# Kernel tuning notes

Measured on AMD Instinct MI355X. Metric: run time of the kernel, lower is better.

The kernel has to match this reference:

```python
import jax, jax.numpy as jnp
import numpy as np

N = 100000   # nodes
E = 1600000  # directed edges (avg degree 16)
IN = 256     # input feature dim


def _gcn_norm(src, dst, n):
    # PyG gcn_norm with unit edge weights: deg computed on destination,
    # norm = deg^{-1/2}[src] * deg^{-1/2}[dst]
    deg = jax.ops.segment_sum(jnp.ones_like(dst, jnp.float32), dst, num_segments=n)
    dinv = jnp.where(deg > 0, jax.lax.rsqrt(deg), 0.0)
    return dinv[src] * dinv[dst]


def _gcn_conv(x, W, b, src, dst, norm, n):
    h = x @ W                          # [N, out] dense transform first (PyG order)
    msg = norm[:, None] * h[src]       # gather + scale  [E+N, out]
    agg = jax.ops.segment_sum(msg, dst, num_segments=n)  # scatter-add
    return agg + b


def setup_inputs() -> dict:
    key = jax.random.key(0)
    ks = jax.random.split(key, 5)
    x = jax.random.normal(ks[0], (N, IN), jnp.float32)
    edge_index = jax.random.randint(ks[1], (2, E), 0, N, dtype=jnp.int32)
    W1 = jax.random.normal(ks[2], (IN, 64), jnp.float32) * (1.0 / np.sqrt(IN))
    b1 = jnp.zeros((64,), jnp.float32)
    W2 = jax.random.normal(ks[3], (64, 32), jnp.float32) * (1.0 / np.sqrt(64))
    b2 = jnp.zeros((32,), jnp.float32)
    Wlin = jax.random.normal(ks[4], (32, 1), jnp.float32) * (1.0 / np.sqrt(32))
    blin = jnp.zeros((1,), jnp.float32)
    return {"x": x, "edge_index": edge_index, "W1": W1, "b1": b1,
            "W2": W2, "b2": b2, "Wlin": Wlin, "blin": blin}


def reference(x, edge_index, W1, b1, W2, b2, Wlin, blin):
    n = x.shape[0]
    loops = jnp.arange(n, dtype=edge_index.dtype)  # add self-loops (GCNConv default)
    src = jnp.concatenate([edge_index[0], loops])
    dst = jnp.concatenate([edge_index[1], loops])
    norm = _gcn_norm(src, dst, n)                  # same for both layers
    h = jax.nn.relu(_gcn_conv(x, W1, b1, src, dst, norm, n))
    h = jax.nn.relu(_gcn_conv(h, W2, b2, src, dst, norm, n))
    return h @ Wlin + blin
```

## Files before the change

### kernel.cpp

```cpp
#include <hip/hip_runtime.h>
#include <hip/hip_fp16.h>
#include <math.h>


#define BSH 9

typedef _Float16 half8 __attribute__((ext_vector_type(8)));
typedef float floatx4 __attribute__((ext_vector_type(4)));


static __global__ __launch_bounds__(256) void k_bcount(const int* __restrict__ dst,
                                                       int* __restrict__ bkt_cnt,
                                                       int e, int nbkt) {
    __shared__ int sh[256];
    int t = threadIdx.x;
    sh[t] = 0;
    __syncthreads();
    for (int i = blockIdx.x * 256 + t; i < e; i += gridDim.x * 256)
        atomicAdd(&sh[dst[i] >> BSH], 1);
    __syncthreads();
    if (t < nbkt && sh[t]) atomicAdd(&bkt_cnt[t], sh[t]);
}

static __global__ __launch_bounds__(256) void k_bscan(const int* __restrict__ bkt_cnt,
                                                      int* __restrict__ bkt_off,
                                                      int* __restrict__ bkt_cur,
                                                      int nbkt, int e) {
    __shared__ int sh[256];
    int t = threadIdx.x;
    int v = (t < nbkt) ? bkt_cnt[t] : 0;
    sh[t] = v;
    __syncthreads();
    for (int o = 1; o < 256; o <<= 1) {
        int u = (t >= o) ? sh[t - o] : 0;
        __syncthreads();
        sh[t] += u;
        __syncthreads();
    }
    int excl = sh[t] - v;
    if (t < nbkt) { bkt_off[t] = excl; bkt_cur[t] = excl; }
    if (t == 0) bkt_off[nbkt] = e;
}

static __global__ __launch_bounds__(256) void k_bscatter(const int* __restrict__ src,
                                                         const int* __restrict__ dst,
                                                         int* __restrict__ bkt_cur,
                                                         int* __restrict__ bsrc,
                                                         int* __restrict__ bdst,
                                                         int e, int nbkt) {
    __shared__ int ssrc[4096], sdst[4096];
    __shared__ unsigned char sbkt[4096];
    __shared__ int cnt[256], loff[256], lcur[256], gbase[256], sh[256];
    int t  = threadIdx.x;
    int cb = blockIdx.x * 4096;
    int cc = min(4096, e - cb);

    cnt[t] = 0;
    __syncthreads();
    int es[16], ed[16];
    int nv = 0;
    #pragma unroll
    for (int k = 0; k < 16; ++k) {
        int i = cb + k * 256 + t;
        if (i < e) {
            es[nv] = src[i];
            ed[nv] = dst[i];
            atomicAdd(&cnt[ed[nv] >> BSH], 1);
            ++nv;
        }
    }
    __syncthreads();
    int v = cnt[t];
    sh[t] = v;
    __syncthreads();
    for (int o = 1; o < 256; o <<= 1) {
        int u = (t >= o) ? sh[t - o] : 0;
        __syncthreads();
        sh[t] += u;
        __syncthreads();
    }
    loff[t] = sh[t] - v;
    lcur[t] = sh[t] - v;
    if (t < nbkt && v > 0) gbase[t] = atomicAdd(&bkt_cur[t], v);
    __syncthreads();
    for (int k = 0; k < nv; ++k) {
        int b = ed[k] >> BSH;
        int p = atomicAdd(&lcur[b], 1);
        ssrc[p] = es[k];
        sdst[p] = ed[k];
        sbkt[p] = (unsigned char)b;
    }
    __syncthreads();
    for (int i = t; i < cc; i += 256) {
        int b = sbkt[i];
        int g = gbase[b] + (i - loff[b]);
        bsrc[g] = ssrc[i];
        bdst[g] = sdst[i];
    }
}

static __global__ __launch_bounds__(512) void k_bfinal(const int* __restrict__ bkt_off,
                                                       const int* __restrict__ bsrc,
                                                       const int* __restrict__ bdst,
                                                       float* __restrict__ dinv,
                                                       int* __restrict__ offs,
                                                       int* __restrict__ csr_src, int n) {
    __shared__ int cnt[512], sh[512], lcur[512];
    int t = threadIdx.x;
    int base = blockIdx.x << BSH;
    int e0 = bkt_off[blockIdx.x], e1 = bkt_off[blockIdx.x + 1];
    cnt[t] = 0;
    __syncthreads();
    for (int i = e0 + t; i < e1; i += 512) atomicAdd(&cnt[bdst[i] - base], 1);
    __syncthreads();
    int v = cnt[t];
    if (base + t < n) dinv[base + t] = 1.0f / sqrtf((float)(v + 1));
    sh[t] = v;
    __syncthreads();
    for (int o = 1; o < 512; o <<= 1) {
        int u = (t >= o) ? sh[t - o] : 0;
        __syncthreads();
        sh[t] += u;
        __syncthreads();
    }
    int incl = sh[t];
    if (base + t < n) offs[base + t] = e0 + incl;
    lcur[t] = e0 + incl - v;
    __syncthreads();
    for (int i = e0 + t; i < e1; i += 512) {
        int d = bdst[i] - base;
        int p = atomicAdd(&lcur[d], 1);
        csr_src[p] = bsrc[i];
    }
}

static __global__ __launch_bounds__(256) void k_wfrag(const float* __restrict__ W1,
                                                      _Float16* __restrict__ w1f) {
    int t = threadIdx.x;
    for (int idx = t; idx < 2048; idx += 256) {
        int kb = idx >> 8;
        int nt = (idx >> 6) & 3;
        int l  = idx & 63;
        int k0 = kb * 32 + ((l >> 4) << 3);
        int nn = nt * 16 + (l & 15);
        half8 b;
        #pragma unroll
        for (int j = 0; j < 8; ++j) b[j] = (_Float16)W1[(k0 + j) * 64 + nn];
        *(half8*)(w1f + (size_t)idx * 8) = b;
    }
}

static __global__ __launch_bounds__(256) void k_gemm1m(const float* __restrict__ x,
                                                       const _Float16* __restrict__ w1f,
                                                       _Float16* __restrict__ h1f, int n) {
    __shared__ _Float16 Wl[16384];
    int t = threadIdx.x;
    {
        const float4* s = (const float4*)w1f;
        float4* d = (float4*)Wl;
        #pragma unroll
        for (int i = 0; i < 8; ++i) d[t + i * 256] = s[t + i * 256];
    }
    __syncthreads();

    int l = t & 63;
    int w = t >> 6;
    int r0 = blockIdx.x * 128 + w * 32;
    int kq = (l >> 4) << 3;
    int ra0 = r0 + (l & 15);
    int ra1 = ra0 + 16;
    ra0 = ra0 < n ? ra0 : n - 1;
    ra1 = ra1 < n ? ra1 : n - 1;
    const float* p0 = x + (size_t)ra0 * 256 + kq;
    const float* p1 = x + (size_t)ra1 * 256 + kq;

    floatx4 acc[2][4];
    #pragma unroll
    for (int mt = 0; mt < 2; ++mt)
        #pragma unroll
        for (int nt = 0; nt < 4; ++nt)
            acc[mt][nt] = (floatx4){0.f, 0.f, 0.f, 0.f};

    #pragma unroll
    for (int kb = 0; kb < 8; ++kb) {
        float4 u0 = *(const float4*)(p0 + kb * 32);
        float4 u1 = *(const float4*)(p0 + kb * 32 + 4);
        float4 v0 = *(const float4*)(p1 + kb * 32);
        float4 v1 = *(const float4*)(p1 + kb * 32 + 4);
        half8 a0, a1;
        a0[0] = (_Float16)u0.x; a0[1] = (_Float16)u0.y; a0[2] = (_Float16)u0.z; a0[3] = (_Float16)u0.w;
        a0[4] = (_Float16)u1.x; a0[5] = (_Float16)u1.y; a0[6] = (_Float16)u1.z; a0[7] = (_Float16)u1.w;
        a1[0] = (_Float16)v0.x; a1[1] = (_Float16)v0.y; a1[2] = (_Float16)v0.z; a1[3] = (_Float16)v0.w;
        a1[4] = (_Float16)v1.x; a1[5] = (_Float16)v1.y; a1[6] = (_Float16)v1.z; a1[7] = (_Float16)v1.w;
        #pragma unroll
        for (int nt = 0; nt < 4; ++nt) {
            half8 b = *(const half8*)(Wl + ((size_t)(kb * 4 + nt) * 64 + l) * 8);
            acc[0][nt] = __builtin_amdgcn_mfma_f32_16x16x32_f16(a0, b, acc[0][nt], 0, 0, 0);
            acc[1][nt] = __builtin_amdgcn_mfma_f32_16x16x32_f16(a1, b, acc[1][nt], 0, 0, 0);
        }
    }

    int quad = l >> 4;
    int col  = l & 15;
    #pragma unroll
    for (int mt = 0; mt < 2; ++mt) {
        #pragma unroll
        for (int r = 0; r < 4; ++r) {
            int rr = r0 + mt * 16 + quad * 4 + r;
            if (rr < n) {
                _Float16* o = h1f + (size_t)rr * 64 + col;
                #pragma unroll
                for (int nt = 0; nt < 4; ++nt)
                    o[nt * 16] = (_Float16)acc[mt][nt][r];
            }
        }
    }
}


static __global__ __launch_bounds__(256) void k_agg1gemm2(const int* __restrict__ offs,
                                                          const int* __restrict__ csr_src,
                                                          const float* __restrict__ dinv,
                                                          const __half2* __restrict__ h1h,
                                                          const float* __restrict__ b1,
                                                          const float* __restrict__ W2,
                                                          __half* __restrict__ h2h, int n) {
    __shared__ float Wl[64 * 32];
    __shared__ float aggL[8][64];
    int t = threadIdx.x;
    *(float4*)(Wl + t * 4)        = *(const float4*)(W2 + t * 4);
    *(float4*)(Wl + t * 4 + 1024) = *(const float4*)(W2 + t * 4 + 1024);

    int li = t & 31;
    int ni = t >> 5;
    int node  = blockIdx.x * 8 + ni;
    int nodeC = node < n ? node : n - 1;
    int start = nodeC ? offs[nodeC - 1] : 0;
    int end   = offs[nodeC];
    float dd  = dinv[nodeC];
    float2 hf = __half22float2(h1h[(size_t)nodeC * 32 + li]);
    float accx = dd * hf.x, accy = dd * hf.y;

    int j = start;
    for (; j + 3 < end; j += 4) {
        int s0 = csr_src[j], s1 = csr_src[j + 1], s2 = csr_src[j + 2], s3 = csr_src[j + 3];
        float w0 = dinv[s0], w1 = dinv[s1], w2 = dinv[s2], w3 = dinv[s3];
        float2 v0 = __half22float2(h1h[(size_t)s0 * 32 + li]);
        float2 v1 = __half22float2(h1h[(size_t)s1 * 32 + li]);
        float2 v2 = __half22float2(h1h[(size_t)s2 * 32 + li]);
        float2 v3 = __half22float2(h1h[(size_t)s3 * 32 + li]);
        accx += w0 * v0.x + w1 * v1.x + w2 * v2.x + w3 * v3.x;
        accy += w0 * v0.y + w1 * v1.y + w2 * v2.y + w3 * v3.y;
    }
    for (; j < end; ++j) {
        int s = csr_src[j];
        float w = dinv[s];
        float2 v = __half22float2(h1h[(size_t)s * 32 + li]);
        accx += w * v.x;
        accy += w * v.y;
    }
    float2 bb = ((const float2*)b1)[li];
    aggL[ni][2 * li + 0] = fmaxf(dd * accx + bb.x, 0.f);
    aggL[ni][2 * li + 1] = fmaxf(dd * accy + bb.y, 0.f);
    __syncthreads();

    if (node < n) {
        float s = 0.f;
        #pragma unroll
        for (int k = 0; k < 64; ++k) s += aggL[ni][k] * Wl[k * 32 + li];
        h2h[(size_t)node * 32 + li] = __float2half(s);
    }
}


static __global__ __launch_bounds__(256) void k_gather2f(const int* __restrict__ offs,
                                                         const int* __restrict__ csr_src,
                                                         const float* __restrict__ dinv,
                                                         const __half2* __restrict__ h2h,
                                                         const float* __restrict__ b2,
                                                         const float* __restrict__ Wlin,
                                                         const float* __restrict__ blin,
                                                         float* __restrict__ out, int n) {
    int g    = blockIdx.x * 256 + threadIdx.x;
    int node = g >> 4;
    if (node >= n) return;
    int li = g & 15;
    int start = node ? offs[node - 1] : 0;
    int end   = offs[node];
    float dd  = dinv[node];
    float2 hf = __half22float2(h2h[(size_t)node * 16 + li]);
    float accx = dd * hf.x, accy = dd * hf.y;

    int j = start;
    for (; j + 3 < end; j += 4) {
        int s0 = csr_src[j], s1 = csr_src[j + 1], s2 = csr_src[j + 2], s3 = csr_src[j + 3];
        float w0 = dinv[s0], w1 = dinv[s1], w2 = dinv[s2], w3 = dinv[s3];
        float2 v0 = __half22float2(h2h[(size_t)s0 * 16 + li]);
        float2 v1 = __half22float2(h2h[(size_t)s1 * 16 + li]);
        float2 v2 = __half22float2(h2h[(size_t)s2 * 16 + li]);
        float2 v3 = __half22float2(h2h[(size_t)s3 * 16 + li]);
        accx += w0 * v0.x + w1 * v1.x + w2 * v2.x + w3 * v3.x;
        accy += w0 * v0.y + w1 * v1.y + w2 * v2.y + w3 * v3.y;
    }
    for (; j < end; ++j) {
        int s = csr_src[j];
        float w = dinv[s];
        float2 v = __half22float2(h2h[(size_t)s * 16 + li]);
        accx += w * v.x;
        accy += w * v.y;
    }
    float2 bb = ((const float2*)b2)[li];
    float2 wl = ((const float2*)Wlin)[li];
    float val = fmaxf(dd * accx + bb.x, 0.f) * wl.x +
                fmaxf(dd * accy + bb.y, 0.f) * wl.y;
    #pragma unroll
    for (int m = 8; m >= 1; m >>= 1) val += __shfl_xor(val, m);
    if (li == 0) out[node] = val + blin[0];
}

extern "C" void kernel_launch(void* const* d_in, const int* in_sizes, int n_in,
                              void* d_out, int out_size, void* d_ws, size_t ws_size,
                              hipStream_t stream) {
    const float* x    = (const float*)d_in[0];
    const int*   ei   = (const int*)d_in[1];
    const float* W1   = (const float*)d_in[2];
    const float* b1   = (const float*)d_in[3];
    const float* W2   = (const float*)d_in[4];
    const float* b2   = (const float*)d_in[5];
    const float* Wlin = (const float*)d_in[6];
    const float* blin = (const float*)d_in[7];
    float* out = (float*)d_out;

    const int n = in_sizes[0] / 256;
    const int e = in_sizes[1] / 2;
    const int* src = ei;
    const int* dst = ei + e;
    const int nbkt = (n + 511) >> BSH;

    char* wp = (char*)d_ws;
    __half2*  h1h = (__half2*)wp;
    _Float16* h1f = (_Float16*)wp;    wp += (size_t)n * 32 * 4;
    __half*   h2h = (__half*)wp;      wp += (size_t)n * 32 * 2;
    float*    dinv = (float*)wp;      wp += (size_t)n * 4;
    int*      offs = (int*)wp;        wp += (size_t)n * 4;
    int*      csr_src = (int*)wp;     wp += (size_t)e * 4;
    int*      bsrc = (int*)wp;        wp += (size_t)e * 4;
    int*      bdst = (int*)wp;        wp += (size_t)e * 4;
    int*      bkt_cnt = (int*)wp;     wp += 256 * 4;
    int*      bkt_off = (int*)wp;     wp += 257 * 4;
    int*      bkt_cur = (int*)wp;     wp += 256 * 4;
    _Float16* w1f = (_Float16*)wp;

    dim3 B(256);
    hipMemsetAsync(bkt_cnt, 0, (size_t)nbkt * 4, stream);
    k_bcount  <<<256, B, 0, stream>>>(dst, bkt_cnt, e, nbkt);
    k_bscan   <<<1, B, 0, stream>>>(bkt_cnt, bkt_off, bkt_cur, nbkt, e);
    k_bscatter<<<(e + 4095) / 4096, B, 0, stream>>>(src, dst, bkt_cur, bsrc, bdst, e, nbkt);
    k_bfinal  <<<nbkt, 512, 0, stream>>>(bkt_off, bsrc, bdst, dinv, offs, csr_src, n);

    k_wfrag   <<<1, B, 0, stream>>>(W1, w1f);
    k_gemm1m  <<<(n + 127) / 128, B, 0, stream>>>(x, w1f, h1f, n);
    k_agg1gemm2<<<(n + 7) / 8, B, 0, stream>>>(offs, csr_src, dinv, h1h, b1, W2, h2h, n);
    k_gather2f <<<(n * 16 + 255) / 256, B, 0, stream>>>(offs, csr_src, dinv, (const __half2*)h2h,
                                                        b2, Wlin, blin, out, n);
}
```

Baseline: 333.1 us.

## Fuse edge bucketing with first GEMM and use fixed-capacity buckets

Result: faster. 294.9 us (-11.5%).

```diff
diff --git a/kernel.cpp b/kernel.cpp
--- a/kernel.cpp
+++ b/kernel.cpp
@@ -3,136 +3,11 @@
 #include <math.h>
 
 
-#define BSH 9
+#define BSH  9
+#define BCAP 12288
 
 typedef _Float16 half8 __attribute__((ext_vector_type(8)));
 typedef float floatx4 __attribute__((ext_vector_type(4)));
-
-
-static __global__ __launch_bounds__(256) void k_bcount(const int* __restrict__ dst,
-                                                       int* __restrict__ bkt_cnt,
-                                                       int e, int nbkt) {
-    __shared__ int sh[256];
-    int t = threadIdx.x;
-    sh[t] = 0;
-    __syncthreads();
-    for (int i = blockIdx.x * 256 + t; i < e; i += gridDim.x * 256)
-        atomicAdd(&sh[dst[i] >> BSH], 1);
-    __syncthreads();
-    if (t < nbkt && sh[t]) atomicAdd(&bkt_cnt[t], sh[t]);
-}
-
-static __global__ __launch_bounds__(256) void k_bscan(const int* __restrict__ bkt_cnt,
-                                                      int* __restrict__ bkt_off,
-                                                      int* __restrict__ bkt_cur,
-                                                      int nbkt, int e) {
-    __shared__ int sh[256];
-    int t = threadIdx.x;
-    int v = (t < nbkt) ? bkt_cnt[t] : 0;
-    sh[t] = v;
-    __syncthreads();
-    for (int o = 1; o < 256; o <<= 1) {
-        int u = (t >= o) ? sh[t - o] : 0;
-        __syncthreads();
-        sh[t] += u;
-        __syncthreads();
-    }
-    int excl = sh[t] - v;
-    if (t < nbkt) { bkt_off[t] = excl; bkt_cur[t] = excl; }
-    if (t == 0) bkt_off[nbkt] = e;
-}
-
-static __global__ __launch_bounds__(256) void k_bscatter(const int* __restrict__ src,
-                                                         const int* __restrict__ dst,
-                                                         int* __restrict__ bkt_cur,
-                                                         int* __restrict__ bsrc,
-                                                         int* __restrict__ bdst,
-                                                         int e, int nbkt) {
-    __shared__ int ssrc[4096], sdst[4096];
-    __shared__ unsigned char sbkt[4096];
-    __shared__ int cnt[256], loff[256], lcur[256], gbase[256], sh[256];
-    int t  = threadIdx.x;
-    int cb = blockIdx.x * 4096;
-    int cc = min(4096, e - cb);
-
-    cnt[t] = 0;
-    __syncthreads();
-    int es[16], ed[16];
-    int nv = 0;
-    #pragma unroll
-    for (int k = 0; k < 16; ++k) {
-        int i = cb + k * 256 + t;
-        if (i < e) {
-            es[nv] = src[i];
-            ed[nv] = dst[i];
-            atomicAdd(&cnt[ed[nv] >> BSH], 1);
-            ++nv;
-        }
-    }
-    __syncthreads();
-    int v = cnt[t];
-    sh[t] = v;
-    __syncthreads();
-    for (int o = 1; o < 256; o <<= 1) {
-        int u = (t >= o) ? sh[t - o] : 0;
-        __syncthreads();
-        sh[t] += u;
-        __syncthreads();
-    }
-    loff[t] = sh[t] - v;
-    lcur[t] = sh[t] - v;
-    if (t < nbkt && v > 0) gbase[t] = atomicAdd(&bkt_cur[t], v);
-    __syncthreads();
-    for (int k = 0; k < nv; ++k) {
-        int b = ed[k] >> BSH;
-        int p = atomicAdd(&lcur[b], 1);
-        ssrc[p] = es[k];
-        sdst[p] = ed[k];
-        sbkt[p] = (unsigned char)b;
-    }
-    __syncthreads();
-    for (int i = t; i < cc; i += 256) {
-        int b = sbkt[i];
-        int g = gbase[b] + (i - loff[b]);
-        bsrc[g] = ssrc[i];
-        bdst[g] = sdst[i];
-    }
-}
-
-static __global__ __launch_bounds__(512) void k_bfinal(const int* __restrict__ bkt_off,
-                                                       const int* __restrict__ bsrc,
-                                                       const int* __restrict__ bdst,
-                                                       float* __restrict__ dinv,
-                                                       int* __restrict__ offs,
-                                                       int* __restrict__ csr_src, int n) {
-    __shared__ int cnt[512], sh[512], lcur[512];
-    int t = threadIdx.x;
-    int base = blockIdx.x << BSH;
-    int e0 = bkt_off[blockIdx.x], e1 = bkt_off[blockIdx.x + 1];
-    cnt[t] = 0;
-    __syncthreads();
-    for (int i = e0 + t; i < e1; i += 512) atomicAdd(&cnt[bdst[i] - base], 1);
-    __syncthreads();
-    int v = cnt[t];
-    if (base + t < n) dinv[base + t] = 1.0f / sqrtf((float)(v + 1));
-    sh[t] = v;
-    __syncthreads();
-    for (int o = 1; o < 512; o <<= 1) {
-        int u = (t >= o) ? sh[t - o] : 0;
-        __syncthreads();
-        sh[t] += u;
-        __syncthreads();
-    }
-    int incl = sh[t];
-    if (base + t < n) offs[base + t] = e0 + incl;
-    lcur[t] = e0 + incl - v;
-    __syncthreads();
-    for (int i = e0 + t; i < e1; i += 512) {
-        int d = bdst[i] - base;
-        int p = atomicAdd(&lcur[d], 1);
-        csr_src[p] = bsrc[i];
-    }
-}
 
 static __global__ __launch_bounds__(256) void k_wfrag(const float* __restrict__ W1,
                                                       _Float16* __restrict__ w1f) {
@@ -150,73 +25,169 @@
     }
 }
 
-static __global__ __launch_bounds__(256) void k_gemm1m(const float* __restrict__ x,
-                                                       const _Float16* __restrict__ w1f,
-                                                       _Float16* __restrict__ h1f, int n) {
-    __shared__ _Float16 Wl[16384];
+static __global__ __launch_bounds__(256) void k_fat(const float* __restrict__ x,
+                                                    const _Float16* __restrict__ w1f,
+                                                    _Float16* __restrict__ h1f,
+                                                    const int* __restrict__ src,
+                                                    const int* __restrict__ dst,
+                                                    int* __restrict__ bkt_cnt,
+                                                    int* __restrict__ epack,
+                                                    int n, int e, int nScat) {
+    __shared__ alignas(16) char smem[32768];
     int t = threadIdx.x;
-    {
-        const float4* s = (const float4*)w1f;
-        float4* d = (float4*)Wl;
-        #pragma unroll
-        for (int i = 0; i < 8; ++i) d[t + i * 256] = s[t + i * 256];
-    }
-    __syncthreads();
-
-    int l = t & 63;
-    int w = t >> 6;
-    int r0 = blockIdx.x * 128 + w * 32;
-    int kq = (l >> 4) << 3;
-    int ra0 = r0 + (l & 15);
-    int ra1 = ra0 + 16;
-    ra0 = ra0 < n ? ra0 : n - 1;
-    ra1 = ra1 < n ? ra1 : n - 1;
-    const float* p0 = x + (size_t)ra0 * 256 + kq;
-    const float* p1 = x + (size_t)ra1 * 256 + kq;
-
-    floatx4 acc[2][4];
-    #pragma unroll
-    for (int mt = 0; mt < 2; ++mt)
-        #pragma unroll
-        for (int nt = 0; nt < 4; ++nt)
-            acc[mt][nt] = (floatx4){0.f, 0.f, 0.f, 0.f};
-
-    #pragma unroll
-    for (int kb = 0; kb < 8; ++kb) {
-        float4 u0 = *(const float4*)(p0 + kb * 32);
-        float4 u1 = *(const float4*)(p0 + kb * 32 + 4);
-        float4 v0 = *(const float4*)(p1 + kb * 32);
-        float4 v1 = *(const float4*)(p1 + kb * 32 + 4);
-        half8 a0, a1;
-        a0[0] = (_Float16)u0.x; a0[1] = (_Float16)u0.y; a0[2] = (_Float16)u0.z; a0[3] = (_Float16)u0.w;
-        a0[4] = (_Float16)u1.x; a0[5] = (_Float16)u1.y; a0[6] = (_Float16)u1.z; a0[7] = (_Float16)u1.w;
-        a1[0] = (_Float16)v0.x; a1[1] = (_Float16)v0.y; a1[2] = (_Float16)v0.z; a1[3] = (_Float16)v0.w;
-        a1[4] = (_Float16)v1.x; a1[5] = (_Float16)v1.y; a1[6] = (_Float16)v1.z; a1[7] = (_Float16)v1.w;
-        #pragma unroll
-        for (int nt = 0; nt < 4; ++nt) {
-            half8 b = *(const half8*)(Wl + ((size_t)(kb * 4 + nt) * 64 + l) * 8);
-            acc[0][nt] = __builtin_amdgcn_mfma_f32_16x16x32_f16(a0, b, acc[0][nt], 0, 0, 0);
-            acc[1][nt] = __builtin_amdgcn_mfma_f32_16x16x32_f16(a1, b, acc[1][nt], 0, 0, 0);
-        }
-    }
-
-    int quad = l >> 4;
-    int col  = l & 15;
-    #pragma unroll
-    for (int mt = 0; mt < 2; ++mt) {
-        #pragma unroll
-        for (int r = 0; r < 4; ++r) {
-            int rr = r0 + mt * 16 + quad * 4 + r;
-            if (rr < n) {
-                _Float16* o = h1f + (size_t)rr * 64 + col;
-                #pragma unroll
-                for (int nt = 0; nt < 4; ++nt)
-                    o[nt * 16] = (_Float16)acc[mt][nt][r];
+
+    if ((int)blockIdx.x < nScat) {
+        int*           sp    = (int*)smem;
+        unsigned char* sbkt  = (unsigned char*)(smem + 16384);
+        int*           cnt   = (int*)(smem + 20480);
+        int*           loff  = (int*)(smem + 21504);
+        int*           lcur  = (int*)(smem + 22528);
+        int*           gbase = (int*)(smem + 23552);
+        int*           sh    = (int*)(smem + 24576);
+        int cb = blockIdx.x * 4096;
+        int cc = min(4096, e - cb);
+
+        cnt[t] = 0;
+        __syncthreads();
+        int ep[16]; unsigned char eb[16];
+        int nv = 0;
+        #pragma unroll
+        for (int k = 0; k < 16; ++k) {
+            int i = cb + k * 256 + t;
+            if (i < e) {
+                int s = src[i], d = dst[i];
+                int b = d >> BSH;
+                ep[nv] = ((d & 511) << 17) | s;
+                eb[nv] = (unsigned char)b;
+                atomicAdd(&cnt[b], 1);
+                ++nv;
             }
         }
-    }
-}
-
+        __syncthreads();
+        int v = cnt[t];
+        sh[t] = v;
+        __syncthreads();
+        for (int o = 1; o < 256; o <<= 1) {
+            int u = (t >= o) ? sh[t - o] : 0;
+            __syncthreads();
+            sh[t] += u;
+            __syncthreads();
+        }
+        loff[t] = sh[t] - v;
+        lcur[t] = sh[t] - v;
+        if (v > 0) gbase[t] = t * BCAP + atomicAdd(&bkt_cnt[t], v);
+        __syncthreads();
+        for (int k = 0; k < nv; ++k) {
+            int b = eb[k];
+            int p = atomicAdd(&lcur[b], 1);
+            sp[p] = ep[k];
+            sbkt[p] = (unsigned char)b;
+        }
+        __syncthreads();
+        for (int i = t; i < cc; i += 256) {
+            int b = sbkt[i];
+            epack[gbase[b] + (i - loff[b])] = sp[i];
+        }
+    } else {
+        _Float16* Wl = (_Float16*)smem;
+        {
+            const float4* s = (const float4*)w1f;
+            float4* d = (float4*)smem;
+            #pragma unroll
+            for (int i = 0; i < 8; ++i) d[t + i * 256] = s[t + i * 256];
+        }
+        __syncthreads();
+
+        int l = t & 63;
+        int w = t >> 6;
+        int r0 = (blockIdx.x - nScat) * 128 + w * 32;
+        int kq = (l >> 4) << 3;
+        int ra0 = r0 + (l & 15);
+        int ra1 = ra0 + 16;
+        ra0 = ra0 < n ? ra0 : n - 1;
+        ra1 = ra1 < n ? ra1 : n - 1;
+        const float* p0 = x + (size_t)ra0 * 256 + kq;
+        const float* p1 = x + (size_t)ra1 * 256 + kq;
+
+        floatx4 acc[2][4];
+        #pragma unroll
+        for (int mt = 0; mt < 2; ++mt)
+            #pragma unroll
+            for (int nt = 0; nt < 4; ++nt)
+                acc[mt][nt] = (floatx4){0.f, 0.f, 0.f, 0.f};
+
+        #pragma unroll
+        for (int kb = 0; kb < 8; ++kb) {
+            float4 u0 = *(const float4*)(p0 + kb * 32);
+            float4 u1 = *(const float4*)(p0 + kb * 32 + 4);
+            float4 v0 = *(const float4*)(p1 + kb * 32);
+            float4 v1 = *(const float4*)(p1 + kb * 32 + 4);
+            half8 a0, a1;
+            a0[0] = (_Float16)u0.x; a0[1] = (_Float16)u0.y; a0[2] = (_Float16)u0.z; a0[3] = (_Float16)u0.w;
+            a0[4] = (_Float16)u1.x; a0[5] = (_Float16)u1.y; a0[6] = (_Float16)u1.z; a0[7] = (_Float16)u1.w;
+            a1[0] = (_Float16)v0.x; a1[1] = (_Float16)v0.y; a1[2] = (_Float16)v0.z; a1[3] = (_Float16)v0.w;
+            a1[4] = (_Float16)v1.x; a1[5] = (_Float16)v1.y; a1[6] = (_Float16)v1.z; a1[7] = (_Float16)v1.w;
+            #pragma unroll
+            for (int nt = 0; nt < 4; ++nt) {
+                half8 b = *(const half8*)(Wl + ((size_t)(kb * 4 + nt) * 64 + l) * 8);
+                acc[0][nt] = __builtin_amdgcn_mfma_f32_16x16x32_f16(a0, b, acc[0][nt], 0, 0, 0);
+                acc[1][nt] = __builtin_amdgcn_mfma_f32_16x16x32_f16(a1, b, acc[1][nt], 0, 0, 0);
+            }
+        }
+
+        int quad = l >> 4;
+        int col  = l & 15;
+        #pragma unroll
+        for (int mt = 0; mt < 2; ++mt) {
+            #pragma unroll
+            for (int r = 0; r < 4; ++r) {
+                int rr = r0 + mt * 16 + quad * 4 + r;
+                if (rr < n) {
+                    _Float16* o = h1f + (size_t)rr * 64 + col;
+                    #pragma unroll
+                    for (int nt = 0; nt < 4; ++nt)
+                        o[nt * 16] = (_Float16)acc[mt][nt][r];
+                }
+            }
+        }
+    }
+}
+
+static __global__ __launch_bounds__(512) void k_bfinal(const int* __restrict__ bkt_cnt,
+                                                       const int* __restrict__ epack,
+                                                       float* __restrict__ dinv,
+                                                       int* __restrict__ offs,
+                                                       int* __restrict__ csr_src, int n) {
+    __shared__ int cnt[512], sh[512], lcur[512];
+    int t = threadIdx.x;
+    int base = blockIdx.x << BSH;
+    int e0 = blockIdx.x * BCAP;
+    int e1 = e0 + bkt_cnt[blockIdx.x];
+    cnt[t] = 0;
+    __syncthreads();
+    for (int i = e0 + t; i < e1; i += 512) atomicAdd(&cnt[epack[i] >> 17], 1);
+    __syncthreads();
+    int v = cnt[t];
+    if (base + t < n) dinv[base + t] = 1.0f / sqrtf((float)(v + 1));
+    sh[t] = v;
+    __syncthreads();
+    for (int o = 1; o < 512; o <<= 1) {
+        int u = (t >= o) ? sh[t - o] : 0;
+        __syncthreads();
+        sh[t] += u;
+        __syncthreads();
+    }
+    int incl = sh[t];
+    if (base + t < n) offs[base + t] = e0 + incl;
+    lcur[t] = e0 + incl - v;
+    __syncthreads();
+    for (int i = e0 + t; i < e1; i += 512) {
+        int p = epack[i];
+        int d = p >> 17;
+        int pos = atomicAdd(&lcur[d], 1);
+        csr_src[pos] = p & 0x1FFFF;
+    }
+}
 
 static __global__ __launch_bounds__(256) void k_agg1gemm2(const int* __restrict__ offs,
                                                           const int* __restrict__ csr_src,
@@ -235,7 +206,7 @@
     int ni = t >> 5;
     int node  = blockIdx.x * 8 + ni;
     int nodeC = node < n ? node : n - 1;
-    int start = nodeC ? offs[nodeC - 1] : 0;
+    int start = (nodeC & 511) ? offs[nodeC - 1] : (nodeC >> BSH) * BCAP;
     int end   = offs[nodeC];
     float dd  = dinv[nodeC];
     float2 hf = __half22float2(h1h[(size_t)nodeC * 32 + li]);
@@ -271,7 +242,6 @@
         h2h[(size_t)node * 32 + li] = __float2half(s);
     }
 }
-
 
 static __global__ __launch_bounds__(256) void k_gather2f(const int* __restrict__ offs,
                                                          const int* __restrict__ csr_src,
@@ -285,7 +255,7 @@
     int node = g >> 4;
     if (node >= n) return;
     int li = g & 15;
-    int start = node ? offs[node - 1] : 0;
+    int start = (node & 511) ? offs[node - 1] : (node >> BSH) * BCAP;
     int end   = offs[node];
     float dd  = dinv[node];
     float2 hf = __half22float2(h2h[(size_t)node * 16 + li]);
@@ -335,7 +305,9 @@
     const int e = in_sizes[1] / 2;
     const int* src = ei;
     const int* dst = ei + e;
-    const int nbkt = (n + 511) >> BSH;
+    const int nbkt  = (n + (1 << BSH) - 1) >> BSH;
+    const int nScat = (e + 4095) / 4096;
+    const int nGemm = (n + 127) / 128;
 
     char* wp = (char*)d_ws;
     __half2*  h1h = (__half2*)wp;
@@ -343,23 +315,16 @@
     __half*   h2h = (__half*)wp;      wp += (size_t)n * 32 * 2;
     float*    dinv = (float*)wp;      wp += (size_t)n * 4;
     int*      offs = (int*)wp;        wp += (size_t)n * 4;
-    int*      csr_src = (int*)wp;     wp += (size_t)e * 4;
-    int*      bsrc = (int*)wp;        wp += (size_t)e * 4;
-    int*      bdst = (int*)wp;        wp += (size_t)e * 4;
+    int*      csr_src = (int*)wp;     wp += (size_t)nbkt * BCAP * 4;
+    int*      epack = (int*)wp;       wp += (size_t)nbkt * BCAP * 4;
     int*      bkt_cnt = (int*)wp;     wp += 256 * 4;
-    int*      bkt_off = (int*)wp;     wp += 257 * 4;
-    int*      bkt_cur = (int*)wp;     wp += 256 * 4;
     _Float16* w1f = (_Float16*)wp;
 
     dim3 B(256);
-    hipMemsetAsync(bkt_cnt, 0, (size_t)nbkt * 4, stream);
-    k_bcount  <<<256, B, 0, stream>>>(dst, bkt_cnt, e, nbkt);
-    k_bscan   <<<1, B, 0, stream>>>(bkt_cnt, bkt_off, bkt_cur, nbkt, e);
-    k_bscatter<<<(e + 4095) / 4096, B, 0, stream>>>(src, dst, bkt_cur, bsrc, bdst, e, nbkt);
-    k_bfinal  <<<nbkt, 512, 0, stream>>>(bkt_off, bsrc, bdst, dinv, offs, csr_src, n);
-
-    k_wfrag   <<<1, B, 0, stream>>>(W1, w1f);
-    k_gemm1m  <<<(n + 127) / 128, B, 0, stream>>>(x, w1f, h1f, n);
+    hipMemsetAsync(bkt_cnt, 0, 256 * 4, stream);
+    k_wfrag <<<1, B, 0, stream>>>(W1, w1f);
+    k_fat   <<<nScat + nGemm, B, 0, stream>>>(x, w1f, h1f, src, dst, bkt_cnt, epack, n, e, nScat);
+    k_bfinal<<<nbkt, 512, 0, stream>>>(bkt_cnt, epack, dinv, offs, csr_src, n);
     k_agg1gemm2<<<(n + 7) / 8, B, 0, stream>>>(offs, csr_src, dinv, h1h, b1, W2, h2h, n);
     k_gather2f <<<(n * 16 + 255) / 256, B, 0, stream>>>(offs, csr_src, dinv, (const __half2*)h2h,
                                                         b2, Wlin, blin, out, n);
```
